# Kernel optimization log

Measured on AMD Instinct MI355X. Metric: run time of the kernel, lower is better.

The kernel has to match this reference:

```python
import jax, jax.numpy as jnp
import numpy as np

PATCH = 768
POS = 64
HID = 512
B, N = 8, 2048


def setup_inputs() -> dict:
    key = jax.random.key(0)
    ks = jax.random.split(key, 8)
    d_in = PATCH + POS
    s = 1.0 / np.sqrt(d_in)
    return {
        "patches": jax.random.normal(ks[0], (B, N, PATCH), jnp.float32),
        "positions": jax.random.normal(ks[1], (B, N, POS), jnp.float32),
        "Wq": jax.random.uniform(ks[2], (d_in, HID), jnp.float32, -s, s),
        "bq": jax.random.uniform(ks[3], (HID,), jnp.float32, -s, s),
        "Wk": jax.random.uniform(ks[4], (d_in, HID), jnp.float32, -s, s),
        "bk": jax.random.uniform(ks[5], (d_in and HID,), jnp.float32, -s, s),
        "Wv": jax.random.uniform(ks[6], (d_in, HID), jnp.float32, -s, s),
        "bv": jax.random.uniform(ks[7], (HID,), jnp.float32, -s, s),
    }


def reference(patches, positions, Wq, bq, Wk, bk, Wv, bv):
    # concat patch features with positional features: [B, N, PATCH+POS]
    x = jnp.concatenate([patches, positions], axis=-1)
    Q = x @ Wq + bq  # [B, N, HID]
    K = x @ Wk + bk
    V = x @ Wv + bv
    scale = jnp.sqrt(jnp.asarray(HID, x.dtype))
    scores = jnp.einsum("bnd,bmd->bnm", Q, K) / scale  # [B, N, N]
    weights = jax.nn.softmax(scores, axis=-1)
    return jnp.einsum("bnm,bmd->bnd", weights, V)  # [B, N, HID]
```

## Files before the change

kernel.cpp:

```cpp
#include <hip/hip_runtime.h>
#include <hip/hip_bf16.h>
#include <math.h>

typedef __hip_bfloat16 bf16;
typedef __attribute__((ext_vector_type(4))) float f32x4;
typedef __attribute__((ext_vector_type(8))) short s16x8;

typedef const __attribute__((address_space(1))) void gvoid_t;
typedef __attribute__((address_space(3))) void lvoid_t;

__device__ __forceinline__ void gload16(const void* g, void* l) {
  __builtin_amdgcn_global_load_lds((gvoid_t*)g, (lvoid_t*)l, 16, 0, 0);
}
__device__ __forceinline__ float b2f(unsigned short u) {
  return __uint_as_float(((unsigned int)u) << 16);
}
__device__ __forceinline__ unsigned short f2b(float f) {
  bf16 h = __float2bfloat16(f);
  return *(unsigned short*)&h;
}

__global__ __launch_bounds__(256) void prep_x(const float* __restrict__ patches,
                                              const float* __restrict__ positions,
                                              bf16* __restrict__ xb) {
  const long long row = blockIdx.x;
  const int c = threadIdx.x;
  const bool lo = (c < 192);
  const bool hi = (c >= 192) && (c < 208);
  const float* src = lo ? (patches + row * 768 + c * 4)
                        : (positions + row * 64 + (c - 192) * 4);
  if (lo || hi) {
    float4 v = *(const float4*)src;
    const int dst = lo ? (c * 4) : (768 + (c - 192) * 4);
    uint2 w;
    w.x = (unsigned int)f2b(v.x) | ((unsigned int)f2b(v.y) << 16);
    w.y = (unsigned int)f2b(v.z) | ((unsigned int)f2b(v.w) << 16);
    *(uint2*)(xb + row * 832 + dst) = w;
  }
}

__global__ __launch_bounds__(256) void prep_w(const float* __restrict__ Wq,
                                              const float* __restrict__ Wk,
                                              const float* __restrict__ Wv,
                                              bf16* __restrict__ Wt) {
  __shared__ float tile[32][33];
  const int z = blockIdx.z;
  const float* W = (z == 0) ? Wq : (z == 1) ? Wk : Wv;
  bf16* T = Wt + (long long)z * 512 * 832;
  const int n0 = blockIdx.x * 32;
  const int k0 = blockIdx.y * 32;
  const int tx = threadIdx.x, ty = threadIdx.y;
  #pragma unroll
  for (int i = 0; i < 32; i += 8)
    tile[ty + i][tx] = W[(long long)(k0 + ty + i) * 512 + n0 + tx];
  __syncthreads();
  #pragma unroll
  for (int i = 0; i < 32; i += 8)
    T[(long long)(n0 + ty + i) * 832 + k0 + tx] = __float2bfloat16(tile[tx][ty + i]);
}

__global__ __launch_bounds__(256) void gemm_qkv(
    const bf16* __restrict__ xb, const bf16* __restrict__ Wt,
    const float* __restrict__ bq, const float* __restrict__ bk,
    const float* __restrict__ bv,
    bf16* __restrict__ qk, bf16* __restrict__ vt) {
  __shared__ bf16 As[128 * 64];
  __shared__ bf16 Bs[128 * 64];
  const int tid = threadIdx.x;
  const int wave = tid >> 6, lane = tid & 63;
  const int llo = lane & 15, lhi = lane >> 4;
  const int wm = wave >> 1, wn = wave & 1;

  const unsigned int lin = blockIdx.x;
  const unsigned int xcd = lin & 7u, idx = lin >> 3;
  const unsigned int g = xcd * 192u + idx;
  const unsigned int bm_t = g / 12u;
  const unsigned int bn_t = g - bm_t * 12u;
  const int row0 = (int)bm_t * 128;
  const int col0 = (int)bn_t * 128;
  const int z = col0 >> 9;

  f32x4 acc[4][4] = {};

  for (int kt = 0; kt < 832; kt += 64) {
    #pragma unroll
    for (int i = 0; i < 4; i++) {
      const int c = i * 256 + tid;
      const int r = c >> 3, cc = c & 7;
      const int kk = (cc ^ (r & 7)) << 3;
      gload16(xb + ((long long)(row0 + r) * 832 + kt + kk),
              (char*)As + (long long)(i * 256 + wave * 64) * 16);
      gload16(Wt + ((long long)(col0 + r) * 832 + kt + kk),
              (char*)Bs + (long long)(i * 256 + wave * 64) * 16);
    }
    __syncthreads();
    #pragma unroll
    for (int k0 = 0; k0 < 64; k0 += 32) {
      const int xk = ((((k0 >> 3) + lhi) ^ (llo & 7)) << 3);
      s16x8 af[4], bfr[4];
      #pragma unroll
      for (int mf = 0; mf < 4; mf++)
        af[mf] = *(const s16x8*)&As[(wm * 64 + mf * 16 + llo) * 64 + xk];
      #pragma unroll
      for (int nf = 0; nf < 4; nf++)
        bfr[nf] = *(const s16x8*)&Bs[(wn * 64 + nf * 16 + llo) * 64 + xk];
      #pragma unroll
      for (int mf = 0; mf < 4; mf++)
        #pragma unroll
        for (int nf = 0; nf < 4; nf++)
          acc[mf][nf] = __builtin_amdgcn_mfma_f32_16x16x32_bf16(
              af[mf], bfr[nf], acc[mf][nf], 0, 0, 0);
    }
    __syncthreads();
  }

  if (z < 2) {
    const float* bias = z ? bk : bq;
    bf16* outp = qk + (long long)z * 16384 * 512;
    #pragma unroll
    for (int mf = 0; mf < 4; mf++)
      #pragma unroll
      for (int nf = 0; nf < 4; nf++) {
        const int c = (col0 & 511) + wn * 64 + nf * 16 + llo;
        const int grow0 = row0 + wm * 64 + mf * 16 + lhi * 4;
        const float bb = bias[c];
        #pragma unroll
        for (int r = 0; r < 4; r++)
          outp[(long long)(grow0 + r) * 512 + c] =
              __float2bfloat16(acc[mf][nf][r] + bb);
      }
  } else {
    #pragma unroll
    for (int mf = 0; mf < 4; mf++)
      #pragma unroll
      for (int nf = 0; nf < 4; nf++) {
        const int c = (col0 & 511) + wn * 64 + nf * 16 + llo;
        const int grow0 = row0 + wm * 64 + mf * 16 + lhi * 4;
        const int b = grow0 >> 11, j = grow0 & 2047;
        const float bb = bv[c];
        uint2 w;
        w.x = (unsigned int)f2b(acc[mf][nf][0] + bb) |
              ((unsigned int)f2b(acc[mf][nf][1] + bb) << 16);
        w.y = (unsigned int)f2b(acc[mf][nf][2] + bb) |
              ((unsigned int)f2b(acc[mf][nf][3] + bb) << 16);
        *(uint2*)(vt + (long long)b * 512 * 2048 + (long long)c * 2048 + j) = w;
      }
  }
}

__global__ __launch_bounds__(256) void gemm_scores(const bf16* __restrict__ qk,
                                                   bf16* __restrict__ S) {
  __shared__ bf16 As[128 * 64];
  __shared__ bf16 Bs[128 * 64];
  const int tid = threadIdx.x;
  const int wave = tid >> 6, lane = tid & 63;
  const int llo = lane & 15, lhi = lane >> 4;
  const int wm = wave >> 1, wn = wave & 1;

  const unsigned int lin = blockIdx.x;
  const unsigned int xcd = lin & 7u, idx = lin >> 3;
  const unsigned int g = xcd * 256u + idx;
  const int b = (int)(g >> 8);
  const unsigned int rem = g & 255u;
  const int row0 = (int)(rem >> 4) * 128;
  const int col0 = (int)(rem & 15u) * 128;

  const bf16* Ab = qk + (long long)b * 2048 * 512;
  const bf16* Bb = qk + (long long)16384 * 512 + (long long)b * 2048 * 512;

  f32x4 acc[4][4] = {};
  for (int kt = 0; kt < 512; kt += 64) {
    #pragma unroll
    for (int i = 0; i < 4; i++) {
      const int c = i * 256 + tid;
      const int r = c >> 3, cc = c & 7;
      const int kk = (cc ^ (r & 7)) << 3;
      gload16(Ab + ((long long)(row0 + r) * 512 + kt + kk),
              (char*)As + (long long)(i * 256 + wave * 64) * 16);
      gload16(Bb + ((long long)(col0 + r) * 512 + kt + kk),
              (char*)Bs + (long long)(i * 256 + wave * 64) * 16);
    }
    __syncthreads();
    #pragma unroll
    for (int k0 = 0; k0 < 64; k0 += 32) {
      const int xk = ((((k0 >> 3) + lhi) ^ (llo & 7)) << 3);
      s16x8 af[4], bfr[4];
      #pragma unroll
      for (int mf = 0; mf < 4; mf++)
        af[mf] = *(const s16x8*)&As[(wm * 64 + mf * 16 + llo) * 64 + xk];
      #pragma unroll
      for (int nf = 0; nf < 4; nf++)
        bfr[nf] = *(const s16x8*)&Bs[(wn * 64 + nf * 16 + llo) * 64 + xk];
      #pragma unroll
      for (int mf = 0; mf < 4; mf++)
        #pragma unroll
        for (int nf = 0; nf < 4; nf++)
          acc[mf][nf] = __builtin_amdgcn_mfma_f32_16x16x32_bf16(
              af[mf], bfr[nf], acc[mf][nf], 0, 0, 0);
    }
    __syncthreads();
  }

  bf16* Sb = S + (long long)b * 2048 * 2048;
  const float alpha = 0.044194173824159216f;
  #pragma unroll
  for (int mf = 0; mf < 4; mf++)
    #pragma unroll
    for (int nf = 0; nf < 4; nf++) {
      const int gcol = col0 + wn * 64 + nf * 16 + llo;
      const int grow0 = row0 + wm * 64 + mf * 16 + lhi * 4;
      #pragma unroll
      for (int r = 0; r < 4; r++)
        Sb[(long long)(grow0 + r) * 2048 + gcol] =
            __float2bfloat16(acc[mf][nf][r] * alpha);
    }
}

__global__ __launch_bounds__(256) void softmax_rows(bf16* __restrict__ S) {
  const long long row = blockIdx.x;
  bf16* p = S + row * 2048;
  const int tid = threadIdx.x;
  const int lane = tid & 63, wave = tid >> 6;
  __shared__ float redm[4], reds[4];
  uint4 raw = *(const uint4*)(p + tid * 8);
  const unsigned short* us = (const unsigned short*)&raw;
  float v[8];
  float mx = -3.0e38f;
  #pragma unroll
  for (int i = 0; i < 8; i++) {
    v[i] = b2f(us[i]);
    mx = fmaxf(mx, v[i]);
  }
  #pragma unroll
  for (int off = 32; off > 0; off >>= 1) mx = fmaxf(mx, __shfl_xor(mx, off, 64));
  if (lane == 0) redm[wave] = mx;
  __syncthreads();
  mx = fmaxf(fmaxf(redm[0], redm[1]), fmaxf(redm[2], redm[3]));
  float s = 0.f;
  #pragma unroll
  for (int i = 0; i < 8; i++) {
    v[i] = __expf(v[i] - mx);
    s += v[i];
  }
  #pragma unroll
  for (int off = 32; off > 0; off >>= 1) s += __shfl_xor(s, off, 64);
  if (lane == 0) reds[wave] = s;
  __syncthreads();
  const float inv = 1.0f / (reds[0] + reds[1] + reds[2] + reds[3]);
  uint4 o;
  o.x = (unsigned int)f2b(v[0] * inv) | ((unsigned int)f2b(v[1] * inv) << 16);
  o.y = (unsigned int)f2b(v[2] * inv) | ((unsigned int)f2b(v[3] * inv) << 16);
  o.z = (unsigned int)f2b(v[4] * inv) | ((unsigned int)f2b(v[5] * inv) << 16);
  o.w = (unsigned int)f2b(v[6] * inv) | ((unsigned int)f2b(v[7] * inv) << 16);
  *(uint4*)(p + tid * 8) = o;
}

__global__ __launch_bounds__(256) void gemm_pv(const bf16* __restrict__ S,
                                               const bf16* __restrict__ vt,
                                               float* __restrict__ out) {
  __shared__ bf16 As[64 * 64];
  __shared__ bf16 Bs[128 * 64];
  const int tid = threadIdx.x;
  const int wave = tid >> 6, lane = tid & 63;
  const int llo = lane & 15, lhi = lane >> 4;
  const int wm = wave >> 1, wn = wave & 1;

  const unsigned int lin = blockIdx.x;
  const unsigned int xcd = lin & 7u, idx = lin >> 3;
  const unsigned int g = xcd * 128u + idx;
  const int b = (int)(g >> 7);
  const unsigned int rem = g & 127u;
  const int row0 = (int)(rem >> 2) * 64;
  const int col0 = (int)(rem & 3u) * 128;

  const bf16* Ab = S + (long long)b * 2048 * 2048;
  const bf16* Bb = vt + (long long)b * 512 * 2048;

  f32x4 acc[2][4] = {};
  for (int kt = 0; kt < 2048; kt += 64) {
    #pragma unroll
    for (int i = 0; i < 2; i++) {
      const int c = i * 256 + tid;
      const int r = c >> 3, cc = c & 7;
      const int kk = (cc ^ (r & 7)) << 3;
      gload16(Ab + ((long long)(row0 + r) * 2048 + kt + kk),
              (char*)As + (long long)(i * 256 + wave * 64) * 16);
    }
    #pragma unroll
    for (int i = 0; i < 4; i++) {
      const int c = i * 256 + tid;
      const int r = c >> 3, cc = c & 7;
      const int kk = (cc ^ (r & 7)) << 3;
      gload16(Bb + ((long long)(col0 + r) * 2048 + kt + kk),
              (char*)Bs + (long long)(i * 256 + wave * 64) * 16);
    }
    __syncthreads();
    #pragma unroll
    for (int k0 = 0; k0 < 64; k0 += 32) {
      const int xk = ((((k0 >> 3) + lhi) ^ (llo & 7)) << 3);
      s16x8 af[2], bfr[4];
      #pragma unroll
      for (int mf = 0; mf < 2; mf++)
        af[mf] = *(const s16x8*)&As[(wm * 32 + mf * 16 + llo) * 64 + xk];
      #pragma unroll
      for (int nf = 0; nf < 4; nf++)
        bfr[nf] = *(const s16x8*)&Bs[(wn * 64 + nf * 16 + llo) * 64 + xk];
      #pragma unroll
      for (int mf = 0; mf < 2; mf++)
        #pragma unroll
        for (int nf = 0; nf < 4; nf++)
          acc[mf][nf] = __builtin_amdgcn_mfma_f32_16x16x32_bf16(
              af[mf], bfr[nf], acc[mf][nf], 0, 0, 0);
    }
    __syncthreads();
  }

  float* Ob = out + (long long)b * 2048 * 512;
  #pragma unroll
  for (int mf = 0; mf < 2; mf++)
    #pragma unroll
    for (int nf = 0; nf < 4; nf++) {
      const int gcol = col0 + wn * 64 + nf * 16 + llo;
      const int grow0 = row0 + wm * 32 + mf * 16 + lhi * 4;
      #pragma unroll
      for (int r = 0; r < 4; r++)
        Ob[(long long)(grow0 + r) * 512 + gcol] = acc[mf][nf][r];
    }
}

extern "C" void kernel_launch(void* const* d_in, const int* in_sizes, int n_in,
                              void* d_out, int out_size, void* d_ws, size_t ws_size,
                              hipStream_t stream) {
  const float* patches = (const float*)d_in[0];
  const float* positions = (const float*)d_in[1];
  const float* Wq = (const float*)d_in[2];
  const float* bq = (const float*)d_in[3];
  const float* Wk = (const float*)d_in[4];
  const float* bk = (const float*)d_in[5];
  const float* Wv = (const float*)d_in[6];
  const float* bv = (const float*)d_in[7];
  float* out = (float*)d_out;

  if (ws_size < 147259392u) return;

  char* ws = (char*)d_ws;
  bf16* Wt = (bf16*)(ws);
  bf16* xb = (bf16*)(ws + 2555904);
  bf16* qk = (bf16*)(ws + 29818880);
  bf16* vt = (bf16*)(ws + 63373312);
  bf16* S  = (bf16*)(ws + 80150528);

  prep_x<<<16384, 256, 0, stream>>>(patches, positions, xb);
  prep_w<<<dim3(16, 26, 3), dim3(32, 8), 0, stream>>>(Wq, Wk, Wv, Wt);
  gemm_qkv<<<1536, 256, 0, stream>>>(xb, Wt, bq, bk, bv, qk, vt);
  gemm_scores<<<2048, 256, 0, stream>>>(qk, S);
  softmax_rows<<<16384, 256, 0, stream>>>(S);
  gemm_pv<<<1024, 256, 0, stream>>>(S, vt, out);
}
```

Measured before the change: 281.4 us.

## Load B operand fragments directly from global into registers, enlarge PV tile

```diff
diff --git a/kernel.cpp b/kernel.cpp
--- a/kernel.cpp
+++ b/kernel.cpp
@@ -65,7 +65,6 @@
     const float* __restrict__ bv,
     bf16* __restrict__ qk, bf16* __restrict__ vt) {
   __shared__ bf16 As[128 * 64];
-  __shared__ bf16 Bs[128 * 64];
   const int tid = threadIdx.x;
   const int wave = tid >> 6, lane = tid & 63;
   const int llo = lane & 15, lhi = lane >> 4;
@@ -80,6 +79,11 @@
   const int col0 = (int)bn_t * 128;
   const int z = col0 >> 9;
 
+  const bf16* brow[4];
+  #pragma unroll
+  for (int nf = 0; nf < 4; nf++)
+    brow[nf] = Wt + (long long)(col0 + wn * 64 + nf * 16 + llo) * 832 + lhi * 8;
+
   f32x4 acc[4][4] = {};
 
   for (int kt = 0; kt < 832; kt += 64) {
@@ -90,26 +94,27 @@
       const int kk = (cc ^ (r & 7)) << 3;
       gload16(xb + ((long long)(row0 + r) * 832 + kt + kk),
               (char*)As + (long long)(i * 256 + wave * 64) * 16);
-      gload16(Wt + ((long long)(col0 + r) * 832 + kt + kk),
-              (char*)Bs + (long long)(i * 256 + wave * 64) * 16);
-    }
-    __syncthreads();
-    #pragma unroll
-    for (int k0 = 0; k0 < 64; k0 += 32) {
-      const int xk = ((((k0 >> 3) + lhi) ^ (llo & 7)) << 3);
-      s16x8 af[4], bfr[4];
+    }
+    s16x8 bfr[2][4];
+    #pragma unroll
+    for (int h = 0; h < 2; h++)
+      #pragma unroll
+      for (int nf = 0; nf < 4; nf++)
+        bfr[h][nf] = *(const s16x8*)(brow[nf] + kt + h * 32);
+    __syncthreads();
+    #pragma unroll
+    for (int h = 0; h < 2; h++) {
+      const int xk = ((((h * 4) + lhi) ^ (llo & 7)) << 3);
+      s16x8 af[4];
       #pragma unroll
       for (int mf = 0; mf < 4; mf++)
         af[mf] = *(const s16x8*)&As[(wm * 64 + mf * 16 + llo) * 64 + xk];
-      #pragma unroll
-      for (int nf = 0; nf < 4; nf++)
-        bfr[nf] = *(const s16x8*)&Bs[(wn * 64 + nf * 16 + llo) * 64 + xk];
       #pragma unroll
       for (int mf = 0; mf < 4; mf++)
         #pragma unroll
         for (int nf = 0; nf < 4; nf++)
           acc[mf][nf] = __builtin_amdgcn_mfma_f32_16x16x32_bf16(
-              af[mf], bfr[nf], acc[mf][nf], 0, 0, 0);
+              af[mf], bfr[h][nf], acc[mf][nf], 0, 0, 0);
     }
     __syncthreads();
   }
@@ -151,7 +156,6 @@
 __global__ __launch_bounds__(256) void gemm_scores(const bf16* __restrict__ qk,
                                                    bf16* __restrict__ S) {
   __shared__ bf16 As[128 * 64];
-  __shared__ bf16 Bs[128 * 64];
   const int tid = threadIdx.x;
   const int wave = tid >> 6, lane = tid & 63;
   const int llo = lane & 15, lhi = lane >> 4;
@@ -168,6 +172,11 @@
   const bf16* Ab = qk + (long long)b * 2048 * 512;
   const bf16* Bb = qk + (long long)16384 * 512 + (long long)b * 2048 * 512;
 
+  const bf16* brow[4];
+  #pragma unroll
+  for (int nf = 0; nf < 4; nf++)
+    brow[nf] = Bb + (long long)(col0 + wn * 64 + nf * 16 + llo) * 512 + lhi * 8;
+
   f32x4 acc[4][4] = {};
   for (int kt = 0; kt < 512; kt += 64) {
     #pragma unroll
@@ -177,26 +186,27 @@
       const int kk = (cc ^ (r & 7)) << 3;
       gload16(Ab + ((long long)(row0 + r) * 512 + kt + kk),
               (char*)As + (long long)(i * 256 + wave * 64) * 16);
-      gload16(Bb + ((long long)(col0 + r) * 512 + kt + kk),
-              (char*)Bs + (long long)(i * 256 + wave * 64) * 16);
-    }
-    __syncthreads();
-    #pragma unroll
-    for (int k0 = 0; k0 < 64; k0 += 32) {
-      const int xk = ((((k0 >> 3) + lhi) ^ (llo & 7)) << 3);
-      s16x8 af[4], bfr[4];
+    }
+    s16x8 bfr[2][4];
+    #pragma unroll
+    for (int h = 0; h < 2; h++)
+      #pragma unroll
+      for (int nf = 0; nf < 4; nf++)
+        bfr[h][nf] = *(const s16x8*)(brow[nf] + kt + h * 32);
+    __syncthreads();
+    #pragma unroll
+    for (int h = 0; h < 2; h++) {
+      const int xk = ((((h * 4) + lhi) ^ (llo & 7)) << 3);
+      s16x8 af[4];
       #pragma unroll
       for (int mf = 0; mf < 4; mf++)
         af[mf] = *(const s16x8*)&As[(wm * 64 + mf * 16 + llo) * 64 + xk];
-      #pragma unroll
-      for (int nf = 0; nf < 4; nf++)
-        bfr[nf] = *(const s16x8*)&Bs[(wn * 64 + nf * 16 + llo) * 64 + xk];
       #pragma unroll
       for (int mf = 0; mf < 4; mf++)
         #pragma unroll
         for (int nf = 0; nf < 4; nf++)
           acc[mf][nf] = __builtin_amdgcn_mfma_f32_16x16x32_bf16(
-              af[mf], bfr[nf], acc[mf][nf], 0, 0, 0);
+              af[mf], bfr[h][nf], acc[mf][nf], 0, 0, 0);
     }
     __syncthreads();
   }
@@ -258,8 +268,7 @@
 __global__ __launch_bounds__(256) void gemm_pv(const bf16* __restrict__ S,
                                                const bf16* __restrict__ vt,
                                                float* __restrict__ out) {
-  __shared__ bf16 As[64 * 64];
-  __shared__ bf16 Bs[128 * 64];
+  __shared__ bf16 As[128 * 64];
   const int tid = threadIdx.x;
   const int wave = tid >> 6, lane = tid & 63;
   const int llo = lane & 15, lhi = lane >> 4;
@@ -267,61 +276,59 @@
 
   const unsigned int lin = blockIdx.x;
   const unsigned int xcd = lin & 7u, idx = lin >> 3;
-  const unsigned int g = xcd * 128u + idx;
-  const int b = (int)(g >> 7);
-  const unsigned int rem = g & 127u;
-  const int row0 = (int)(rem >> 2) * 64;
-  const int col0 = (int)(rem & 3u) * 128;
+  const int b = (int)xcd;
+  const int row0 = (int)(idx >> 2) * 128;
+  const int col0 = (int)(idx & 3u) * 128;
 
   const bf16* Ab = S + (long long)b * 2048 * 2048;
   const bf16* Bb = vt + (long long)b * 512 * 2048;
 
-  f32x4 acc[2][4] = {};
+  const bf16* brow[4];
+  #pragma unroll
+  for (int nf = 0; nf < 4; nf++)
+    brow[nf] = Bb + (long long)(col0 + wn * 64 + nf * 16 + llo) * 2048 + lhi * 8;
+
+  f32x4 acc[4][4] = {};
   for (int kt = 0; kt < 2048; kt += 64) {
     #pragma unroll
-    for (int i = 0; i < 2; i++) {
+    for (int i = 0; i < 4; i++) {
       const int c = i * 256 + tid;
       const int r = c >> 3, cc = c & 7;
       const int kk = (cc ^ (r & 7)) << 3;
       gload16(Ab + ((long long)(row0 + r) * 2048 + kt + kk),
               (char*)As + (long long)(i * 256 + wave * 64) * 16);
     }
-    #pragma unroll
-    for (int i = 0; i < 4; i++) {
-      const int c = i * 256 + tid;
-      const int r = c >> 3, cc = c & 7;
-      const int kk = (cc ^ (r & 7)) << 3;
-      gload16(Bb + ((long long)(col0 + r) * 2048 + kt + kk),
-              (char*)Bs + (long long)(i * 256 + wave * 64) * 16);
-    }
-    __syncthreads();
-    #pragma unroll
-    for (int k0 = 0; k0 < 64; k0 += 32) {
-      const int xk = ((((k0 >> 3) + lhi) ^ (llo & 7)) << 3);
-      s16x8 af[2], bfr[4];
-      #pragma unroll
-      for (int mf = 0; mf < 2; mf++)
-        af[mf] = *(const s16x8*)&As[(wm * 32 + mf * 16 + llo) * 64 + xk];
+    s16x8 bfr[2][4];
+    #pragma unroll
+    for (int h = 0; h < 2; h++)
       #pragma unroll
       for (int nf = 0; nf < 4; nf++)
-        bfr[nf] = *(const s16x8*)&Bs[(wn * 64 + nf * 16 + llo) * 64 + xk];
-      #pragma unroll
-      for (int mf = 0; mf < 2; mf++)
+        bfr[h][nf] = *(const s16x8*)(brow[nf] + kt + h * 32);
+    __syncthreads();
+    #pragma unroll
+    for (int h = 0; h < 2; h++) {
+      const int xk = ((((h * 4) + lhi) ^ (llo & 7)) << 3);
+      s16x8 af[4];
+      #pragma unroll
+      for (int mf = 0; mf < 4; mf++)
+        af[mf] = *(const s16x8*)&As[(wm * 64 + mf * 16 + llo) * 64 + xk];
+      #pragma unroll
+      for (int mf = 0; mf < 4; mf++)
         #pragma unroll
         for (int nf = 0; nf < 4; nf++)
           acc[mf][nf] = __builtin_amdgcn_mfma_f32_16x16x32_bf16(
-              af[mf], bfr[nf], acc[mf][nf], 0, 0, 0);
+              af[mf], bfr[h][nf], acc[mf][nf], 0, 0, 0);
     }
     __syncthreads();
   }
 
   float* Ob = out + (long long)b * 2048 * 512;
   #pragma unroll
-  for (int mf = 0; mf < 2; mf++)
+  for (int mf = 0; mf < 4; mf++)
     #pragma unroll
     for (int nf = 0; nf < 4; nf++) {
       const int gcol = col0 + wn * 64 + nf * 16 + llo;
-      const int grow0 = row0 + wm * 32 + mf * 16 + lhi * 4;
+      const int grow0 = row0 + wm * 64 + mf * 16 + lhi * 4;
       #pragma unroll
       for (int r = 0; r < 4; r++)
         Ob[(long long)(grow0 + r) * 512 + gcol] = acc[mf][nf][r];
@@ -355,5 +362,5 @@
   gemm_qkv<<<1536, 256, 0, stream>>>(xb, Wt, bq, bk, bv, qk, vt);
   gemm_scores<<<2048, 256, 0, stream>>>(qk, S);
   softmax_rows<<<16384, 256, 0, stream>>>(S);
-  gemm_pv<<<1024, 256, 0, stream>>>(S, vt, out);
-}
+  gemm_pv<<<512, 256, 0, stream>>>(S, vt, out);
+}
```

Measured after the change: 381.1 us. +35.4%, slower.

## Fuse softmax into score GEMM epilogue with deferred row normalization

Applied to the files above, without the earlier changes.

```diff
diff --git a/kernel.cpp b/kernel.cpp
--- a/kernel.cpp
+++ b/kernel.cpp
@@ -11,9 +11,6 @@
 
 __device__ __forceinline__ void gload16(const void* g, void* l) {
   __builtin_amdgcn_global_load_lds((gvoid_t*)g, (lvoid_t*)l, 16, 0, 0);
-}
-__device__ __forceinline__ float b2f(unsigned short u) {
-  return __uint_as_float(((unsigned int)u) << 16);
 }
 __device__ __forceinline__ unsigned short f2b(float f) {
   bf16 h = __float2bfloat16(f);
@@ -149,7 +146,8 @@
 }
 
 __global__ __launch_bounds__(256) void gemm_scores(const bf16* __restrict__ qk,
-                                                   bf16* __restrict__ S) {
+                                                   bf16* __restrict__ S,
+                                                   float* __restrict__ rowsum) {
   __shared__ bf16 As[128 * 64];
   __shared__ bf16 Bs[128 * 64];
   const int tid = threadIdx.x;
@@ -201,8 +199,16 @@
     __syncthreads();
   }
 
+  const float alpha = 0.044194173824159216f;
+  #pragma unroll
+  for (int mf = 0; mf < 4; mf++)
+    #pragma unroll
+    for (int nf = 0; nf < 4; nf++)
+      #pragma unroll
+      for (int r = 0; r < 4; r++)
+        acc[mf][nf][r] = __expf(acc[mf][nf][r] * alpha);
+
   bf16* Sb = S + (long long)b * 2048 * 2048;
-  const float alpha = 0.044194173824159216f;
   #pragma unroll
   for (int mf = 0; mf < 4; mf++)
     #pragma unroll
@@ -212,51 +218,28 @@
       #pragma unroll
       for (int r = 0; r < 4; r++)
         Sb[(long long)(grow0 + r) * 2048 + gcol] =
-            __float2bfloat16(acc[mf][nf][r] * alpha);
-    }
-}
-
-__global__ __launch_bounds__(256) void softmax_rows(bf16* __restrict__ S) {
-  const long long row = blockIdx.x;
-  bf16* p = S + row * 2048;
-  const int tid = threadIdx.x;
-  const int lane = tid & 63, wave = tid >> 6;
-  __shared__ float redm[4], reds[4];
-  uint4 raw = *(const uint4*)(p + tid * 8);
-  const unsigned short* us = (const unsigned short*)&raw;
-  float v[8];
-  float mx = -3.0e38f;
-  #pragma unroll
-  for (int i = 0; i < 8; i++) {
-    v[i] = b2f(us[i]);
-    mx = fmaxf(mx, v[i]);
-  }
-  #pragma unroll
-  for (int off = 32; off > 0; off >>= 1) mx = fmaxf(mx, __shfl_xor(mx, off, 64));
-  if (lane == 0) redm[wave] = mx;
-  __syncthreads();
-  mx = fmaxf(fmaxf(redm[0], redm[1]), fmaxf(redm[2], redm[3]));
-  float s = 0.f;
-  #pragma unroll
-  for (int i = 0; i < 8; i++) {
-    v[i] = __expf(v[i] - mx);
-    s += v[i];
-  }
-  #pragma unroll
-  for (int off = 32; off > 0; off >>= 1) s += __shfl_xor(s, off, 64);
-  if (lane == 0) reds[wave] = s;
-  __syncthreads();
-  const float inv = 1.0f / (reds[0] + reds[1] + reds[2] + reds[3]);
-  uint4 o;
-  o.x = (unsigned int)f2b(v[0] * inv) | ((unsigned int)f2b(v[1] * inv) << 16);
-  o.y = (unsigned int)f2b(v[2] * inv) | ((unsigned int)f2b(v[3] * inv) << 16);
-  o.z = (unsigned int)f2b(v[4] * inv) | ((unsigned int)f2b(v[5] * inv) << 16);
-  o.w = (unsigned int)f2b(v[6] * inv) | ((unsigned int)f2b(v[7] * inv) << 16);
-  *(uint4*)(p + tid * 8) = o;
+            __float2bfloat16(acc[mf][nf][r]);
+    }
+
+  float* rs = rowsum + (long long)b * 2048;
+  #pragma unroll
+  for (int mf = 0; mf < 4; mf++) {
+    #pragma unroll
+    for (int r = 0; r < 4; r++) {
+      float p = acc[mf][0][r] + acc[mf][1][r] + acc[mf][2][r] + acc[mf][3][r];
+      p += __shfl_xor(p, 1, 64);
+      p += __shfl_xor(p, 2, 64);
+      p += __shfl_xor(p, 4, 64);
+      p += __shfl_xor(p, 8, 64);
+      if (llo == 0)
+        atomicAdd(&rs[row0 + wm * 64 + mf * 16 + lhi * 4 + r], p);
+    }
+  }
 }
 
 __global__ __launch_bounds__(256) void gemm_pv(const bf16* __restrict__ S,
                                                const bf16* __restrict__ vt,
+                                               const float* __restrict__ rowsum,
                                                float* __restrict__ out) {
   __shared__ bf16 As[64 * 64];
   __shared__ bf16 Bs[128 * 64];
@@ -267,11 +250,9 @@
 
   const unsigned int lin = blockIdx.x;
   const unsigned int xcd = lin & 7u, idx = lin >> 3;
-  const unsigned int g = xcd * 128u + idx;
-  const int b = (int)(g >> 7);
-  const unsigned int rem = g & 127u;
-  const int row0 = (int)(rem >> 2) * 64;
-  const int col0 = (int)(rem & 3u) * 128;
+  const int b = (int)xcd;
+  const int row0 = (int)(idx >> 2) * 64;
+  const int col0 = (int)(idx & 3u) * 128;
 
   const bf16* Ab = S + (long long)b * 2048 * 2048;
   const bf16* Bb = vt + (long long)b * 512 * 2048;
@@ -315,17 +296,22 @@
     __syncthreads();
   }
 
+  const float* rs = rowsum + (long long)b * 2048;
   float* Ob = out + (long long)b * 2048 * 512;
   #pragma unroll
-  for (int mf = 0; mf < 2; mf++)
+  for (int mf = 0; mf < 2; mf++) {
+    const int grow0 = row0 + wm * 32 + mf * 16 + lhi * 4;
+    float inv[4];
+    #pragma unroll
+    for (int r = 0; r < 4; r++) inv[r] = 1.0f / rs[grow0 + r];
     #pragma unroll
     for (int nf = 0; nf < 4; nf++) {
       const int gcol = col0 + wn * 64 + nf * 16 + llo;
-      const int grow0 = row0 + wm * 32 + mf * 16 + lhi * 4;
       #pragma unroll
       for (int r = 0; r < 4; r++)
-        Ob[(long long)(grow0 + r) * 512 + gcol] = acc[mf][nf][r];
-    }
+        Ob[(long long)(grow0 + r) * 512 + gcol] = acc[mf][nf][r] * inv[r];
+    }
+  }
 }
 
 extern "C" void kernel_launch(void* const* d_in, const int* in_sizes, int n_in,
@@ -341,7 +327,7 @@
   const float* bv = (const float*)d_in[7];
   float* out = (float*)d_out;
 
-  if (ws_size < 147259392u) return;
+  if (ws_size < 147324928u) return;
 
   char* ws = (char*)d_ws;
   bf16* Wt = (bf16*)(ws);
@@ -349,11 +335,12 @@
   bf16* qk = (bf16*)(ws + 29818880);
   bf16* vt = (bf16*)(ws + 63373312);
   bf16* S  = (bf16*)(ws + 80150528);
-
+  float* rowsum = (float*)(ws + 147259392);
+
+  hipMemsetAsync(rowsum, 0, 16384 * sizeof(float), stream);
   prep_x<<<16384, 256, 0, stream>>>(patches, positions, xb);
   prep_w<<<dim3(16, 26, 3), dim3(32, 8), 0, stream>>>(Wq, Wk, Wv, Wt);
   gemm_qkv<<<1536, 256, 0, stream>>>(xb, Wt, bq, bk, bv, qk, vt);
-  gemm_scores<<<2048, 256, 0, stream>>>(qk, S);
-  softmax_rows<<<16384, 256, 0, stream>>>(S);
-  gemm_pv<<<1024, 256, 0, stream>>>(S, vt, out);
-}
+  gemm_scores<<<2048, 256, 0, stream>>>(qk, S, rowsum);
+  gemm_pv<<<1024, 256, 0, stream>>>(S, vt, rowsum, out);
+}
```

Result: slower. 287.8 us (+2.2%).
